# Optimization experiments

Measured on AMD Instinct MI355X. Metric: run time of the kernel, lower is better.

The kernel has to match this reference:

```python
import jax, jax.numpy as jnp
import numpy as np

N = 50000      # num nodes
D = 128        # hidden_size
H = 2          # num_head
E = 400000     # num edges / metapath instances
L = 4          # metapath length


def setup_inputs() -> dict:
    key = jax.random.key(0)
    k1, k2, k3, k4, k5, k6 = jax.random.split(key, 6)
    node_features = jax.random.normal(k1, (N, D), dtype=jnp.float32)
    edge_index = jax.random.randint(k2, (2, E), 0, N, dtype=jnp.int64)
    metapath_idx = jax.random.randint(k3, (E, L), 0, N, dtype=jnp.int64)
    s = 1.0 / np.sqrt(D)
    Wq = jax.random.normal(k4, (D, H * D), dtype=jnp.float32) * s
    Wk = jax.random.normal(k5, (D, H * D), dtype=jnp.float32) * s
    Wv = jax.random.normal(k6, (D, H * D), dtype=jnp.float32) * s
    return {"node_features": node_features, "edge_index": edge_index,
            "metapath_idx": metapath_idx, "Wq": Wq, "Wk": Wk, "Wv": Wv}


def _segment_softmax(logits, seg, num_segments):
    # numerically stable softmax over edges grouped by destination node
    m = jax.ops.segment_max(logits, seg, num_segments=num_segments)
    m = jnp.where(jnp.isfinite(m), m, jnp.zeros_like(m))
    ex = jnp.exp(logits - m[seg])
    denom = jax.ops.segment_sum(ex, seg, num_segments=num_segments)
    return ex, denom


def reference(node_features, edge_index, metapath_idx, Wq, Wk, Wv):
    n = node_features.shape[0]
    src, dst = edge_index[0], edge_index[1]

    # --- intra-metapath aggregation (mean over path positions) ---
    metapath_feat = node_features[metapath_idx]          # [E, L, D] gather
    agg = jnp.mean(metapath_feat, axis=1)                # [E, D]
    edge_attr = jnp.broadcast_to(agg[:, None, :], (agg.shape[0], H, D))  # heads tiled -> [E, H, D]

    # --- multi-head edge attention (TransformerConv-style with edge features) ---
    q = (node_features @ Wq).reshape(n, H, D)[dst]       # [E, H, D]
    k = (node_features @ Wk).reshape(n, H, D)[src] + edge_attr
    v = (node_features @ Wv).reshape(n, H, D)[src] + edge_attr

    logits = jnp.einsum('ehd,ehd->eh', q, k) / jnp.sqrt(jnp.float32(D))  # [E, H]
    ex, denom = _segment_softmax(logits, dst, n)
    msg = ex[..., None] * v                              # [E, H, D]
    out = jax.ops.segment_sum(msg, dst, num_segments=n)  # [N, H, D]
    out = out / (denom[..., None] + jnp.float32(1e-16))
    return out.reshape(n, H * D)                         # concat heads -> [N, H*D]
```

## Files before the change

### kernel.cpp

```cpp
#include <hip/hip_runtime.h>
#include <hip/hip_bf16.h>
#include <hip/hip_fp8.h>

#define D_ 128
#define H_ 2
#define L_ 4
#define HD_ 256
#define P2L 0.12751743f

typedef __attribute__((ext_vector_type(8))) short bf16x8;
typedef __attribute__((ext_vector_type(4))) float f32x4;
typedef __attribute__((ext_vector_type(2))) float f32x2;

__device__ __forceinline__ unsigned short f2bf(float x) {
    __hip_bfloat16 b = __float2bfloat16(x);
    return *reinterpret_cast<unsigned short*>(&b);
}
__device__ __forceinline__ float bf2f(unsigned short u) {
    return __uint_as_float(((unsigned)u) << 16);
}
__device__ __forceinline__ unsigned char f2fp8(float x) {
    __hip_fp8_e4m3 t(x);
    return (unsigned char)t.__x;
}
__device__ __forceinline__ float fp82f(unsigned u) {
    __hip_fp8_e4m3 t; t.__x = (__hip_fp8_storage_t)u; return (float)t;
}
__device__ __forceinline__ void unpack_il(const uint4 v, float* h0, float* h1) {
    const unsigned short* u = reinterpret_cast<const unsigned short*>(&v);
#pragma unroll
    for (int j = 0; j < 4; ++j) { h0[j] = bf2f(u[2 * j]); h1[j] = bf2f(u[2 * j + 1]); }
}

#define HIST_BLOCKS 512
__global__ __launch_bounds__(256)
void prep_hist_kernel(const float* __restrict__ nf,
                      const float* __restrict__ Wq, const float* __restrict__ Wk,
                      const float* __restrict__ Wv, const int* __restrict__ dst,
                      unsigned short* __restrict__ nfb, unsigned char* __restrict__ nf8,
                      unsigned short* __restrict__ Wb, int* __restrict__ counts,
                      int n4, int E_) {
    const int nfbB = (n4 + 255) / 256;
    const int bid = blockIdx.x;
    if (bid < nfbB) {
        const int i = bid * 256 + threadIdx.x;
        if (i < n4) {
            const float4 v = reinterpret_cast<const float4*>(nf)[i];
            ushort4 o;
            o.x = f2bf(v.x); o.y = f2bf(v.y); o.z = f2bf(v.z); o.w = f2bf(v.w);
            reinterpret_cast<ushort4*>(nfb)[i] = o;
            const unsigned p8 = (unsigned)f2fp8(v.x) | ((unsigned)f2fp8(v.y) << 8) |
                                ((unsigned)f2fp8(v.z) << 16) | ((unsigned)f2fp8(v.w) << 24);
            reinterpret_cast<unsigned*>(nf8)[i] = p8;
        }
    } else if (bid < nfbB + 384) {
        const int b = bid - nfbB;
        const int n = b * 2 + (threadIdx.x >> 7);
        const int k = threadIdx.x & 127;
        const float* W = (n < 256) ? Wq : (n < 512) ? Wk : Wv;
        const int c = n & 255;
        Wb[(size_t)n * 128 + k] = f2bf(W[(size_t)k * HD_ + c]);
    } else {
        const int b = bid - nfbB - 384;
        const int nquad = E_ >> 2;
        for (int i = b * 256 + threadIdx.x; i < nquad; i += HIST_BLOCKS * 256) {
            const int4 d4 = reinterpret_cast<const int4*>(dst)[i];
            atomicAdd(&counts[d4.x], 1);
            atomicAdd(&counts[d4.y], 1);
            atomicAdd(&counts[d4.z], 1);
            atomicAdd(&counts[d4.w], 1);
        }
        if (b == 0 && (int)threadIdx.x < (E_ & 3))
            atomicAdd(&counts[dst[(E_ & ~3) + threadIdx.x]], 1);
    }
}

__global__ __launch_bounds__(256)
void qkv_scan_kernel(const unsigned short* __restrict__ nfb,
                     const unsigned short* __restrict__ Wb,
                     unsigned short* __restrict__ Qil,
                     unsigned short* __restrict__ KVil,
                     const int* __restrict__ counts,
                     int* __restrict__ offs, int* __restrict__ blksum,
                     int n_nodes, int qkv_blocks) {
    __shared__ unsigned short sS[32][264];
    __shared__ int sdata[256];

    if ((int)blockIdx.x >= qkv_blocks) {
        const int bid = blockIdx.x - qkv_blocks;
        const int t = threadIdx.x;
        const int base = bid * 1024;
        int v[4]; int sum = 0;
#pragma unroll
        for (int j = 0; j < 4; ++j) {
            int idx = base + t * 4 + j;
            v[j] = (idx < n_nodes) ? counts[idx] : 0;
            sum += v[j];
        }
        sdata[t] = sum;
        __syncthreads();
        for (int off = 1; off < 256; off <<= 1) {
            int x = (t >= off) ? sdata[t - off] : 0;
            __syncthreads();
            sdata[t] += x;
            __syncthreads();
        }
        if (t == 255) blksum[bid] = sdata[255];
        int run = sdata[t] - sum;
#pragma unroll
        for (int j = 0; j < 4; ++j) {
            int idx = base + t * 4 + j;
            if (idx < n_nodes) offs[idx] = run;
            run += v[j];
        }
        return;
    }

    const int tid  = threadIdx.x;
    const int lane = tid & 63;
    const int wv   = tid >> 6;
    const int m0   = blockIdx.x * 32;
    const int r16  = lane & 15;
    const int kg   = lane >> 4;

    bf16x8 afrag[2][4];
#pragma unroll
    for (int ms = 0; ms < 2; ++ms) {
        int arow = m0 + ms * 16 + r16;
        if (arow >= n_nodes) arow = n_nodes - 1;
        const unsigned short* aptr = nfb + (size_t)arow * D_ + kg * 8;
#pragma unroll
        for (int kb = 0; kb < 4; ++kb)
            afrag[ms][kb] = *reinterpret_cast<const bf16x8*>(aptr + kb * 32);
    }

    for (int p = 0; p < 3; ++p) {
#pragma unroll
        for (int j = 0; j < 4; ++j) {
            const int n0 = p * 256 + (wv * 4 + j) * 16;
            const unsigned short* bptr = Wb + (size_t)(n0 + r16) * D_ + kg * 8;
            bf16x8 b0 = *reinterpret_cast<const bf16x8*>(bptr);
            bf16x8 b1 = *reinterpret_cast<const bf16x8*>(bptr + 32);
            bf16x8 b2 = *reinterpret_cast<const bf16x8*>(bptr + 64);
            bf16x8 b3 = *reinterpret_cast<const bf16x8*>(bptr + 96);
            f32x4 acc0 = {0.f, 0.f, 0.f, 0.f};
            f32x4 acc1 = {0.f, 0.f, 0.f, 0.f};
            acc0 = __builtin_amdgcn_mfma_f32_16x16x32_bf16(afrag[0][0], b0, acc0, 0, 0, 0);
            acc1 = __builtin_amdgcn_mfma_f32_16x16x32_bf16(afrag[1][0], b0, acc1, 0, 0, 0);
            acc0 = __builtin_amdgcn_mfma_f32_16x16x32_bf16(afrag[0][1], b1, acc0, 0, 0, 0);
            acc1 = __builtin_amdgcn_mfma_f32_16x16x32_bf16(afrag[1][1], b1, acc1, 0, 0, 0);
            acc0 = __builtin_amdgcn_mfma_f32_16x16x32_bf16(afrag[0][2], b2, acc0, 0, 0, 0);
            acc1 = __builtin_amdgcn_mfma_f32_16x16x32_bf16(afrag[1][2], b2, acc1, 0, 0, 0);
            acc0 = __builtin_amdgcn_mfma_f32_16x16x32_bf16(afrag[0][3], b3, acc0, 0, 0, 0);
            acc1 = __builtin_amdgcn_mfma_f32_16x16x32_bf16(afrag[1][3], b3, acc1, 0, 0, 0);

            const int ln = (n0 & 255) + r16;
            const int il = ((ln & 127) << 1) | ((ln >> 7) & 1);
#pragma unroll
            for (int jj = 0; jj < 4; ++jj) {
                sS[kg * 4 + jj][il]      = f2bf(acc0[jj]);
                sS[16 + kg * 4 + jj][il] = f2bf(acc1[jj]);
            }
        }
        __syncthreads();
        for (int i = tid; i < 32 * 64; i += 256) {
            const int r = i >> 6, c4 = i & 63;
            const int node = m0 + r;
            if (node < n_nodes) {
                const uint2 val = *reinterpret_cast<const uint2*>(&sS[r][c4 * 4]);
                if (p == 0)
                    *reinterpret_cast<uint2*>(&Qil[(size_t)node * HD_ + c4 * 4]) = val;
                else if (p == 1)
                    *reinterpret_cast<uint2*>(&KVil[(size_t)node * 512 + c4 * 4]) = val;
                else
                    *reinterpret_cast<uint2*>(&KVil[(size_t)node * 512 + 256 + c4 * 4]) = val;
            }
        }
        __syncthreads();
    }
}

__global__ __launch_bounds__(64)
void scan2_kernel(int* __restrict__ blksum, int nblk) {
    const int lane = threadIdx.x;
    int carry = 0;
    for (int base = 0; base < nblk; base += 64) {
        const int idx = base + lane;
        int v = (idx < nblk) ? blksum[idx] : 0;
        int inc = v;
#pragma unroll
        for (int off = 1; off < 64; off <<= 1) {
            int x = __shfl_up(inc, off, 64);
            if (lane >= off) inc += x;
        }
        if (idx < nblk) blksum[idx] = carry + inc - v;
        carry += __shfl(inc, 63, 64);
    }
}

__global__ __launch_bounds__(256)
void scatter_kernel(const int* __restrict__ dst, const int* __restrict__ src,
                    const int* __restrict__ mp, int* __restrict__ offs,
                    const int* __restrict__ blksum,
                    int* __restrict__ srcs, int4* __restrict__ mp4s, int E_) {
    for (int i = blockIdx.x * blockDim.x + threadIdx.x; i < E_;
         i += gridDim.x * blockDim.x) {
        const int d = dst[i];
        const int pos = atomicAdd(&offs[d], 1) + blksum[d >> 10];
        srcs[pos] = src[i];
        mp4s[pos] = *reinterpret_cast<const int4*>(&mp[(size_t)i * L_]);
    }
}

__global__ __launch_bounds__(256)
void node_fused_kernel(const unsigned char* __restrict__ nf8,
                       const unsigned short* __restrict__ Qil,
                       const unsigned short* __restrict__ KVil,
                       const int* __restrict__ srcs,
                       const int4* __restrict__ mp4s,
                       const int* __restrict__ ends,
                       const int* __restrict__ blksum,
                       const int* __restrict__ counts,
                       float* __restrict__ out,
                       int n_nodes) {
    const int lane = threadIdx.x & 63;
    const int half = lane >> 5;
    const int sl   = lane & 31;
    const int n = __builtin_amdgcn_readfirstlane(
        (blockIdx.x * blockDim.x + threadIdx.x) >> 6);
    if (n >= n_nodes) return;

    const int deg = counts[n];
    const int end = ends[n] + blksum[n >> 10];
    const int start = end - deg;
    float* o = out + (size_t)n * HD_;

    if (deg == 0) {
        const float4 z = {0.f, 0.f, 0.f, 0.f};
        *reinterpret_cast<float4*>(&o[half * D_ + sl * 4]) = z;
        return;
    }

    float q0[4], q1[4];
    unpack_il(*reinterpret_cast<const uint4*>(&Qil[(size_t)n * HD_ + sl * 8]), q0, q1);

    float m0 = -INFINITY, m1 = -INFINITY;
    float den0 = 0.f, den1 = 0.f;
    float acc0[4] = {0.f, 0.f, 0.f, 0.f};
    float acc1[4] = {0.f, 0.f, 0.f, 0.f};

#if defined(__has_builtin)
#if __has_builtin(__builtin_amdgcn_cvt_pk_f32_fp8)
#define NFROW(node_id, a)                                                              \
    {                                                                                  \
        const unsigned u = *reinterpret_cast<const unsigned*>(                         \
            &nf8[(size_t)(node_id) * D_ + sl * 4]);                                    \
        const f32x2 lo = __builtin_amdgcn_cvt_pk_f32_fp8((int)u, false);               \
        const f32x2 hi = __builtin_amdgcn_cvt_pk_f32_fp8((int)u, true);                \
        a[0] += lo[0]; a[1] += lo[1]; a[2] += hi[0]; a[3] += hi[1];                    \
    }
#endif
#endif
#ifndef NFROW
#define NFROW(node_id, a)                                                              \
    {                                                                                  \
        const unsigned u = *reinterpret_cast<const unsigned*>(                         \
            &nf8[(size_t)(node_id) * D_ + sl * 4]);                                    \
        a[0] += fp82f(u & 0xffu);         a[1] += fp82f((u >> 8) & 0xffu);             \
        a[2] += fp82f((u >> 16) & 0xffu); a[3] += fp82f((u >> 24) & 0xffu);            \
    }
#endif

#define SMUPDATE(p0, p1, v0, v1, a)                                                    \
    {                                                                                  \
        const float l0 = p0 * P2L, l1 = p1 * P2L;                                      \
        if (l0 > m0 || l1 > m1) {                                                      \
            const float nm0 = fmaxf(m0, l0), nm1 = fmaxf(m1, l1);                      \
            const float c0 = exp2f(m0 - nm0), c1 = exp2f(m1 - nm1);                    \
            den0 *= c0; den1 *= c1;                                                    \
            _Pragma("unroll") for (int j = 0; j < 4; ++j) { acc0[j] *= c0; acc1[j] *= c1; } \
            m0 = nm0; m1 = nm1;                                                        \
        }                                                                              \
        const float e0 = exp2f(l0 - m0), e1 = exp2f(l1 - m1);                          \
        den0 += e0; den1 += e1;                                                        \
        _Pragma("unroll") for (int j = 0; j < 4; ++j) {                                \
            acc0[j] = fmaf(e0, v0[j] + a[j], acc0[j]);                                 \
            acc1[j] = fmaf(e1, v1[j] + a[j], acc1[j]);                                 \
        }                                                                              \
    }

    int i = start + half;
    for (; i + 2 < end; i += 4) {
        const int sA = srcs[i];
        const int sB = srcs[i + 2];
        const int4 mA = mp4s[i];
        const int4 mB = mp4s[i + 2];

        const uint4 kuA = *reinterpret_cast<const uint4*>(&KVil[(size_t)sA * 512 + sl * 8]);
        const uint4 vuA = *reinterpret_cast<const uint4*>(&KVil[(size_t)sA * 512 + 256 + sl * 8]);
        const uint4 kuB = *reinterpret_cast<const uint4*>(&KVil[(size_t)sB * 512 + sl * 8]);
        const uint4 vuB = *reinterpret_cast<const uint4*>(&KVil[(size_t)sB * 512 + 256 + sl * 8]);

        float aA[4] = {0.f, 0.f, 0.f, 0.f};
        float aB[4] = {0.f, 0.f, 0.f, 0.f};
        NFROW(mA.x, aA); NFROW(mA.y, aA); NFROW(mA.z, aA); NFROW(mA.w, aA);
        NFROW(mB.x, aB); NFROW(mB.y, aB); NFROW(mB.z, aB); NFROW(mB.w, aB);
#pragma unroll
        for (int j = 0; j < 4; ++j) { aA[j] *= 0.25f; aB[j] *= 0.25f; }

        float k0A[4], k1A[4], v0A[4], v1A[4];
        float k0B[4], k1B[4], v0B[4], v1B[4];
        unpack_il(kuA, k0A, k1A); unpack_il(vuA, v0A, v1A);
        unpack_il(kuB, k0B, k1B); unpack_il(vuB, v0B, v1B);

        float p0A = 0.f, p1A = 0.f, p0B = 0.f, p1B = 0.f;
#pragma unroll
        for (int j = 0; j < 4; ++j) {
            p0A = fmaf(q0[j], k0A[j] + aA[j], p0A);
            p1A = fmaf(q1[j], k1A[j] + aA[j], p1A);
            p0B = fmaf(q0[j], k0B[j] + aB[j], p0B);
            p1B = fmaf(q1[j], k1B[j] + aB[j], p1B);
        }
#pragma unroll
        for (int off = 1; off < 32; off <<= 1) {
            p0A += __shfl_xor(p0A, off, 64);
            p1A += __shfl_xor(p1A, off, 64);
            p0B += __shfl_xor(p0B, off, 64);
            p1B += __shfl_xor(p1B, off, 64);
        }
        SMUPDATE(p0A, p1A, v0A, v1A, aA);
        SMUPDATE(p0B, p1B, v0B, v1B, aB);
    }
    for (; i < end; i += 2) {
        const int s = srcs[i];
        const int4 mm = mp4s[i];
        const uint4 ku = *reinterpret_cast<const uint4*>(&KVil[(size_t)s * 512 + sl * 8]);
        const uint4 vu = *reinterpret_cast<const uint4*>(&KVil[(size_t)s * 512 + 256 + sl * 8]);
        float a[4] = {0.f, 0.f, 0.f, 0.f};
        NFROW(mm.x, a); NFROW(mm.y, a); NFROW(mm.z, a); NFROW(mm.w, a);
#pragma unroll
        for (int j = 0; j < 4; ++j) a[j] *= 0.25f;
        float k0[4], k1[4], v0[4], v1[4];
        unpack_il(ku, k0, k1); unpack_il(vu, v0, v1);
        float p0 = 0.f, p1 = 0.f;
#pragma unroll
        for (int j = 0; j < 4; ++j) {
            p0 = fmaf(q0[j], k0[j] + a[j], p0);
            p1 = fmaf(q1[j], k1[j] + a[j], p1);
        }
#pragma unroll
        for (int off = 1; off < 32; off <<= 1) {
            p0 += __shfl_xor(p0, off, 64);
            p1 += __shfl_xor(p1, off, 64);
        }
        SMUPDATE(p0, p1, v0, v1, a);
    }

    {
        const float M0 = fmaxf(m0, __shfl_xor(m0, 32, 64));
        const float M1 = fmaxf(m1, __shfl_xor(m1, 32, 64));
        const float c0 = exp2f(m0 - M0), c1 = exp2f(m1 - M1);
        den0 *= c0; den1 *= c1;
#pragma unroll
        for (int j = 0; j < 4; ++j) { acc0[j] *= c0; acc1[j] *= c1; }
        den0 += __shfl_xor(den0, 32, 64);
        den1 += __shfl_xor(den1, 32, 64);
#pragma unroll
        for (int j = 0; j < 4; ++j) {
            acc0[j] += __shfl_xor(acc0[j], 32, 64);
            acc1[j] += __shfl_xor(acc1[j], 32, 64);
        }
    }

    const float r0 = 1.f / (den0 + 1e-16f);
    const float r1 = 1.f / (den1 + 1e-16f);
    float4 ov;
    ov.x = half ? acc1[0] * r1 : acc0[0] * r0;
    ov.y = half ? acc1[1] * r1 : acc0[1] * r0;
    ov.z = half ? acc1[2] * r1 : acc0[2] * r0;
    ov.w = half ? acc1[3] * r1 : acc0[3] * r0;
    *reinterpret_cast<float4*>(&o[half * D_ + sl * 4]) = ov;
#undef NFROW
#undef SMUPDATE
}

extern "C" void kernel_launch(void* const* d_in, const int* in_sizes, int n_in,
                              void* d_out, int out_size, void* d_ws, size_t ws_size,
                              hipStream_t stream) {
    const float* nf  = (const float*)d_in[0];
    const int*   ei  = (const int*)d_in[1];
    const int*   mp  = (const int*)d_in[2];
    const float* Wq  = (const float*)d_in[3];
    const float* Wk  = (const float*)d_in[4];
    const float* Wv  = (const float*)d_in[5];
    float* out = (float*)d_out;

    const int N_nodes = in_sizes[0] / D_;
    const int E_edges = in_sizes[1] / 2;
    const int* src = ei;
    const int* dst = ei + E_edges;

    unsigned short* Qil  = (unsigned short*)d_ws;
    unsigned short* KVil = Qil + (size_t)N_nodes * HD_;
    unsigned short* nfb  = KVil + (size_t)N_nodes * 512;
    unsigned char*  nf8  = (unsigned char*)(nfb + (size_t)N_nodes * D_);
    unsigned short* Wb   = (unsigned short*)(nf8 + (size_t)N_nodes * D_);
    int* counts = (int*)(Wb + (size_t)768 * D_);
    int* offs   = counts + N_nodes;
    int* blksum = offs + N_nodes;
    int* srcs   = blksum + 1024;
    uintptr_t p = (uintptr_t)(srcs + E_edges);
    p = (p + 15) & ~(uintptr_t)15;
    int4* mp4s  = (int4*)p;

    const int nblk1 = (N_nodes + 1023) / 1024;
    const int n4 = N_nodes * D_ / 4;
    const int nfb_blocks = (n4 + 255) / 256;
    const int qkv_blocks = (N_nodes + 31) / 32;

    hipMemsetAsync(counts, 0, (size_t)N_nodes * sizeof(int), stream);

    prep_hist_kernel<<<nfb_blocks + 384 + HIST_BLOCKS, 256, 0, stream>>>(
        nf, Wq, Wk, Wv, dst, nfb, nf8, Wb, counts, n4, E_edges);

    qkv_scan_kernel<<<qkv_blocks + nblk1, 256, 0, stream>>>(
        nfb, Wb, Qil, KVil, counts, offs, blksum, N_nodes, qkv_blocks);

    scan2_kernel<<<1, 64, 0, stream>>>(blksum, nblk1);

    scatter_kernel<<<1024, 256, 0, stream>>>(dst, src, mp, offs, blksum, srcs, mp4s, E_edges);

    node_fused_kernel<<<(N_nodes + 3) / 4, 256, 0, stream>>>(
        nf8, Qil, KVil, srcs, mp4s, offs, blksum, counts, out, N_nodes);
}
```

Measured before the change: 212.1 us.

## Overlap QKV GEMM with edge scatter; shrink node kernel blocks to two waves

The count scan now runs as its own kernel ahead of the QKV projection. The QKV GEMM blocks then share a single launch with the CSR scatter blocks, so the scatter overlaps the matmul instead of running in a separate serialized kernel. The node aggregation kernel also moves from 256-thread blocks to 128-thread blocks, two nodes per block, for finer scheduling granularity. Kernel count stays the same, and the scatter's atomics now compete for bandwidth with the GEMM.

```diff
diff --git a/kernel.cpp b/kernel.cpp
--- a/kernel.cpp
+++ b/kernel.cpp
@@ -76,42 +76,74 @@
 }
 
 __global__ __launch_bounds__(256)
-void qkv_scan_kernel(const unsigned short* __restrict__ nfb,
-                     const unsigned short* __restrict__ Wb,
-                     unsigned short* __restrict__ Qil,
-                     unsigned short* __restrict__ KVil,
-                     const int* __restrict__ counts,
-                     int* __restrict__ offs, int* __restrict__ blksum,
-                     int n_nodes, int qkv_blocks) {
+void scan1_kernel(const int* __restrict__ counts, int* __restrict__ offs,
+                  int* __restrict__ blksum, int n) {
+    __shared__ int sdata[256];
+    const int t = threadIdx.x;
+    const int base = blockIdx.x * 1024;
+    int v[4]; int sum = 0;
+#pragma unroll
+    for (int j = 0; j < 4; ++j) {
+        int idx = base + t * 4 + j;
+        v[j] = (idx < n) ? counts[idx] : 0;
+        sum += v[j];
+    }
+    sdata[t] = sum;
+    __syncthreads();
+    for (int off = 1; off < 256; off <<= 1) {
+        int x = (t >= off) ? sdata[t - off] : 0;
+        __syncthreads();
+        sdata[t] += x;
+        __syncthreads();
+    }
+    if (t == 255) blksum[blockIdx.x] = sdata[255];
+    int run = sdata[t] - sum;
+#pragma unroll
+    for (int j = 0; j < 4; ++j) {
+        int idx = base + t * 4 + j;
+        if (idx < n) offs[idx] = run;
+        run += v[j];
+    }
+}
+
+__global__ __launch_bounds__(64)
+void scan2_kernel(int* __restrict__ blksum, int nblk) {
+    const int lane = threadIdx.x;
+    int carry = 0;
+    for (int base = 0; base < nblk; base += 64) {
+        const int idx = base + lane;
+        int v = (idx < nblk) ? blksum[idx] : 0;
+        int inc = v;
+#pragma unroll
+        for (int off = 1; off < 64; off <<= 1) {
+            int x = __shfl_up(inc, off, 64);
+            if (lane >= off) inc += x;
+        }
+        if (idx < nblk) blksum[idx] = carry + inc - v;
+        carry += __shfl(inc, 63, 64);
+    }
+}
+
+#define SCAT_BLOCKS 1024
+__global__ __launch_bounds__(256)
+void qkv_scatter_kernel(const unsigned short* __restrict__ nfb,
+                        const unsigned short* __restrict__ Wb,
+                        unsigned short* __restrict__ Qil,
+                        unsigned short* __restrict__ KVil,
+                        const int* __restrict__ dst, const int* __restrict__ src,
+                        const int* __restrict__ mp, int* __restrict__ offs,
+                        const int* __restrict__ blksum,
+                        int* __restrict__ srcs, int4* __restrict__ mp4s,
+                        int n_nodes, int E_, int qkv_blocks) {
     __shared__ unsigned short sS[32][264];
-    __shared__ int sdata[256];
 
     if ((int)blockIdx.x >= qkv_blocks) {
-        const int bid = blockIdx.x - qkv_blocks;
-        const int t = threadIdx.x;
-        const int base = bid * 1024;
-        int v[4]; int sum = 0;
-#pragma unroll
-        for (int j = 0; j < 4; ++j) {
-            int idx = base + t * 4 + j;
-            v[j] = (idx < n_nodes) ? counts[idx] : 0;
-            sum += v[j];
-        }
-        sdata[t] = sum;
-        __syncthreads();
-        for (int off = 1; off < 256; off <<= 1) {
-            int x = (t >= off) ? sdata[t - off] : 0;
-            __syncthreads();
-            sdata[t] += x;
-            __syncthreads();
-        }
-        if (t == 255) blksum[bid] = sdata[255];
-        int run = sdata[t] - sum;
-#pragma unroll
-        for (int j = 0; j < 4; ++j) {
-            int idx = base + t * 4 + j;
-            if (idx < n_nodes) offs[idx] = run;
-            run += v[j];
+        const int b = blockIdx.x - qkv_blocks;
+        for (int i = b * 256 + threadIdx.x; i < E_; i += SCAT_BLOCKS * 256) {
+            const int d = dst[i];
+            const int pos = atomicAdd(&offs[d], 1) + blksum[d >> 10];
+            srcs[pos] = src[i];
+            mp4s[pos] = *reinterpret_cast<const int4*>(&mp[(size_t)i * L_]);
         }
         return;
     }
@@ -180,39 +212,7 @@
     }
 }
 
-__global__ __launch_bounds__(64)
-void scan2_kernel(int* __restrict__ blksum, int nblk) {
-    const int lane = threadIdx.x;
-    int carry = 0;
-    for (int base = 0; base < nblk; base += 64) {
-        const int idx = base + lane;
-        int v = (idx < nblk) ? blksum[idx] : 0;
-        int inc = v;
-#pragma unroll
-        for (int off = 1; off < 64; off <<= 1) {
-            int x = __shfl_up(inc, off, 64);
-            if (lane >= off) inc += x;
-        }
-        if (idx < nblk) blksum[idx] = carry + inc - v;
-        carry += __shfl(inc, 63, 64);
-    }
-}
-
-__global__ __launch_bounds__(256)
-void scatter_kernel(const int* __restrict__ dst, const int* __restrict__ src,
-                    const int* __restrict__ mp, int* __restrict__ offs,
-                    const int* __restrict__ blksum,
-                    int* __restrict__ srcs, int4* __restrict__ mp4s, int E_) {
-    for (int i = blockIdx.x * blockDim.x + threadIdx.x; i < E_;
-         i += gridDim.x * blockDim.x) {
-        const int d = dst[i];
-        const int pos = atomicAdd(&offs[d], 1) + blksum[d >> 10];
-        srcs[pos] = src[i];
-        mp4s[pos] = *reinterpret_cast<const int4*>(&mp[(size_t)i * L_]);
-    }
-}
-
-__global__ __launch_bounds__(256)
+__global__ __launch_bounds__(128)
 void node_fused_kernel(const unsigned char* __restrict__ nf8,
                        const unsigned short* __restrict__ Qil,
                        const unsigned short* __restrict__ KVil,
@@ -227,7 +227,7 @@
     const int half = lane >> 5;
     const int sl   = lane & 31;
     const int n = __builtin_amdgcn_readfirstlane(
-        (blockIdx.x * blockDim.x + threadIdx.x) >> 6);
+        blockIdx.x * 2 + (threadIdx.x >> 6));
     if (n >= n_nodes) return;
 
     const int deg = counts[n];
@@ -423,13 +423,14 @@
     prep_hist_kernel<<<nfb_blocks + 384 + HIST_BLOCKS, 256, 0, stream>>>(
         nf, Wq, Wk, Wv, dst, nfb, nf8, Wb, counts, n4, E_edges);
 
-    qkv_scan_kernel<<<qkv_blocks + nblk1, 256, 0, stream>>>(
-        nfb, Wb, Qil, KVil, counts, offs, blksum, N_nodes, qkv_blocks);
+    scan1_kernel<<<nblk1, 256, 0, stream>>>(counts, offs, blksum, N_nodes);
 
     scan2_kernel<<<1, 64, 0, stream>>>(blksum, nblk1);
 
-    scatter_kernel<<<1024, 256, 0, stream>>>(dst, src, mp, offs, blksum, srcs, mp4s, E_edges);
-
-    node_fused_kernel<<<(N_nodes + 3) / 4, 256, 0, stream>>>(
+    qkv_scatter_kernel<<<qkv_blocks + SCAT_BLOCKS, 256, 0, stream>>>(
+        nfb, Wb, Qil, KVil, dst, src, mp, offs, blksum, srcs, mp4s,
+        N_nodes, E_edges, qkv_blocks);
+
+    node_fused_kernel<<<(N_nodes + 1) / 2, 128, 0, stream>>>(
         nf8, Qil, KVil, srcs, mp4s, offs, blksum, counts, out, N_nodes);
 }
```

Result: faster. 194.0 us (-8.5%).
